# Performance work log

Hardware: AMD Instinct MI355X
Metric: run time of the kernel (lower is better)

## Reference

```python
import jax, jax.numpy as jnp
import numpy as np

SEQ_LEN = 256
VOCAB = 50000
EMBED = 300
PROJ = 200
ATT = 200
CLS = 3
B = 128


def setup_inputs() -> dict:
    key = jax.random.key(0)
    ks = jax.random.split(key, 16)
    s = lambda d: 1.0 / np.sqrt(d)
    return {
        "x1": jax.random.randint(ks[0], (B, SEQ_LEN), 0, VOCAB, dtype=jnp.int32),
        "x2": jax.random.randint(ks[1], (B, SEQ_LEN), 0, VOCAB, dtype=jnp.int32),
        "emb": jax.random.normal(ks[2], (VOCAB, EMBED), jnp.float32),
        # intra-attention forward_product FC (shared for x1/x2 via AUTO_REUSE)
        "Wi": jax.random.normal(ks[3], (EMBED, ATT), jnp.float32) * s(EMBED),
        "bi": jnp.zeros((ATT,), jnp.float32),
        "b_dist": jax.random.normal(ks[4], (1,), jnp.float32) * 0.1,
        # embed-scope projection (input is concat[x, xp] -> 2*EMBED), linear
        "Wp": jax.random.normal(ks[5], (2 * EMBED, PROJ), jnp.float32) * s(2 * EMBED),
        "bp": jnp.zeros((PROJ,), jnp.float32),
        # attent forward_product FC (shared)
        "Wa": jax.random.normal(ks[6], (PROJ, ATT), jnp.float32) * s(PROJ),
        "ba": jnp.zeros((ATT,), jnp.float32),
        # compare FC (shared, dim = input dim = 2*PROJ)
        "Wc": jax.random.normal(ks[7], (2 * PROJ, 2 * PROJ), jnp.float32) * s(2 * PROJ),
        "bc": jnp.zeros((2 * PROJ,), jnp.float32),
        # aggregate FC -> class logits (linear)
        "Wg": jax.random.normal(ks[8], (4 * PROJ, CLS), jnp.float32) * s(4 * PROJ),
        "bg": jnp.zeros((CLS,), jnp.float32),
    }


def _seq_mask(x):
    # tf.count_nonzero + tf.sequence_mask -> [B, L, 1] float mask
    size = jnp.sum((x != 0).astype(jnp.float32), axis=1)  # [B]
    m = (jnp.arange(SEQ_LEN)[None, :] < size[:, None]).astype(jnp.float32)
    return m[:, :, None]


def _intra(x, Wi, bi, b_dist):
    # forward_product on (x, x): relu FC then bilinear product -> [B, L, L]
    f = jax.nn.relu(x @ Wi + bi)
    att = jnp.einsum("bid,bjd->bij", f, f)
    idx = jnp.arange(SEQ_LEN)
    dist = jnp.abs(idx[None, :] - idx[:, None])
    bias = b_dist[0] * (dist >= 10).astype(jnp.float32)  # [L, L]
    xp = jnp.einsum("bik,bkj->bij", jax.nn.softmax(att + bias[None], axis=2), x)
    return jnp.concatenate([x, xp], axis=2)  # [B, L, 2*EMBED]


def reference(x1, x2, emb, Wi, bi, b_dist, Wp, bp, Wa, ba, Wc, bc, Wg, bg):
    mask1, mask2 = _seq_mask(x1), _seq_mask(x2)  # [B, L, 1]

    # embedding lookup with L2-normalized table
    emb_n = emb / jnp.linalg.norm(emb, axis=1, keepdims=True)
    e1, e2 = emb_n[x1], emb_n[x2]  # [B, L, EMBED]

    # intra-attention (distance-biased self alignment), doubles feature dim
    h1 = _intra(e1, Wi, bi, b_dist)
    h2 = _intra(e2, Wi, bi, b_dist)

    # linear projection to PROJ
    p1 = h1 @ Wp + bp  # [B, L, PROJ]
    p2 = h2 @ Wp + bp

    # attent: forward_product sim + mask + dual-axis softmax alignments
    a1 = jax.nn.relu(p1 @ Wa + ba)
    a2 = jax.nn.relu(p2 @ Wa + ba)
    sim = jnp.einsum("bid,bjd->bij", a1, a2)  # [B, L, L]
    sim = sim * (mask1 * jnp.swapaxes(mask2, 1, 2))
    alpha = jnp.einsum("bki,bkj->bij", jax.nn.softmax(sim, axis=1), p1)
    beta = jnp.einsum("bik,bkj->bij", jax.nn.softmax(sim, axis=2), p2)

    # compare (shared relu FC)
    v1 = jax.nn.relu(jnp.concatenate([p1, beta], 2) @ Wc + bc)
    v2 = jax.nn.relu(jnp.concatenate([p2, alpha], 2) @ Wc + bc)

    # aggregate: masked sum pooling + linear classifier
    v1 = jnp.sum(v1 * mask1, axis=1)  # [B, 2*PROJ]
    v2 = jnp.sum(v2 * mask2, axis=1)
    return jnp.concatenate([v1, v2], 1) @ Wg + bg  # [B, CLS]
```

## Files before the change

### kernel.cpp

```cpp
#include <hip/hip_runtime.h>
#include <math.h>

#define LSEQ 256
#define NB   128

typedef unsigned short u16;
typedef unsigned int   u32;
typedef __attribute__((ext_vector_type(8))) short bf16x8;
typedef __attribute__((ext_vector_type(4))) float f32x4;

static __device__ __forceinline__ u16 f2bf(float x) {
    union { float f; u32 u; } v; v.f = x;
    const u32 r = v.u + 0x7fffu + ((v.u >> 16) & 1u);
    return (u16)(r >> 16);
}
static __device__ __forceinline__ void glds16(const u16* src, u16* dst) {
    __builtin_amdgcn_global_load_lds(
        (const __attribute__((address_space(1))) u32*)src,
        (__attribute__((address_space(3))) u32*)dst, 16, 0, 0);
}

template<int EPI, bool BIAS, bool RELU>
__global__ __launch_bounds__(512)
void gemm(const u16* __restrict__ A, int lda,
          const u16* __restrict__ B, int ldb,
          u16* __restrict__ C, int ldc,
          const float* __restrict__ bias, int Nbias,
          float* __restrict__ pool, const float* __restrict__ pmask,
          int K, int Nwrite)
{
    __shared__ u16 As[128 * 64];
    __shared__ u16 Bs[256 * 64];

    const int m0 = blockIdx.y * 128;
    const int n0 = blockIdx.x * 256;
    const int t = threadIdx.x;
    const int lane = t & 63;
    const int w = t >> 6;
    const int wm = w >> 2;
    const int wn = w & 3;
    const int lr = lane & 15;
    const int lg = lane >> 4;

    f32x4 acc[4][4] = {};

    for (int k0 = 0; k0 < K; k0 += 64) {
#pragma unroll
        for (int i = 0; i < 2; ++i) {
            const int ch = w * 2 + i;
            const int row = (ch << 3) + (lane >> 3);
            const int slot = (lane & 7) ^ (row & 7);
            glds16(A + (long long)(m0 + row) * lda + k0 + (slot << 3), &As[ch << 9]);
        }
#pragma unroll
        for (int i = 0; i < 4; ++i) {
            const int ch = w * 4 + i;
            const int row = (ch << 3) + (lane >> 3);
            const int slot = (lane & 7) ^ (row & 7);
            glds16(B + (long long)(n0 + row) * ldb + k0 + (slot << 3), &Bs[ch << 9]);
        }
        __syncthreads();
#pragma unroll
        for (int kk = 0; kk < 2; ++kk) {
            bf16x8 af[4], bf[4];
#pragma unroll
            for (int mi = 0; mi < 4; ++mi) {
                const int row = wm * 64 + mi * 16 + lr;
                const int slot = ((kk << 2) + lg) ^ (row & 7);
                af[mi] = *reinterpret_cast<const bf16x8*>(&As[row * 64 + (slot << 3)]);
            }
#pragma unroll
            for (int ni = 0; ni < 4; ++ni) {
                const int row = wn * 64 + ni * 16 + lr;
                const int slot = ((kk << 2) + lg) ^ (row & 7);
                bf[ni] = *reinterpret_cast<const bf16x8*>(&Bs[row * 64 + (slot << 3)]);
            }
#pragma unroll
            for (int mi = 0; mi < 4; ++mi)
#pragma unroll
                for (int ni = 0; ni < 4; ++ni)
                    acc[mi][ni] = __builtin_amdgcn_mfma_f32_16x16x32_bf16(
                        af[mi], bf[ni], acc[mi][ni], 0, 0, 0);
        }
        __syncthreads();
    }

    const int rbase = lg << 2;
    if (EPI == 0) {
#pragma unroll
        for (int ni = 0; ni < 4; ++ni) {
            const int gc = n0 + wn * 64 + ni * 16 + lr;
            if (gc >= Nwrite) continue;
            float bcv = 0.f;
            if (BIAS) bcv = (gc < Nbias) ? bias[gc] : 0.f;
#pragma unroll
            for (int mi = 0; mi < 4; ++mi) {
#pragma unroll
                for (int r = 0; r < 4; ++r) {
                    const long long gr = m0 + wm * 64 + mi * 16 + rbase + r;
                    float x = acc[mi][ni][r];
                    if (BIAS) x += bcv;
                    if (RELU) x = fmaxf(x, 0.f);
                    C[gr * ldc + gc] = f2bf(x);
                }
            }
        }
    } else {
        __syncthreads();
        float* pool_s = reinterpret_cast<float*>(As);
        for (int i = t; i < 256; i += 512) pool_s[i] = 0.f;
        __syncthreads();
        const int b_lin = m0 >> 8;
        const int side  = b_lin >> 7;
        const int bb    = b_lin & 127;
        const float* mk = pmask + b_lin * 256 + (m0 & 255);
        float mrow[4][4];
#pragma unroll
        for (int mi = 0; mi < 4; ++mi)
#pragma unroll
            for (int r = 0; r < 4; ++r)
                mrow[mi][r] = mk[wm * 64 + mi * 16 + rbase + r];
#pragma unroll
        for (int ni = 0; ni < 4; ++ni) {
            const int lc = wn * 64 + ni * 16 + lr;
            const int gc = n0 + lc;
            const float bcv = (BIAS && gc < Nbias) ? bias[gc] : 0.f;
            float cs = 0.f;
#pragma unroll
            for (int mi = 0; mi < 4; ++mi)
#pragma unroll
                for (int r = 0; r < 4; ++r)
                    cs += fmaxf(acc[mi][ni][r] + bcv, 0.f) * mrow[mi][r];
            cs += __shfl_xor(cs, 16, 64);
            cs += __shfl_xor(cs, 32, 64);
            if (lg == 0) atomicAdd(&pool_s[lc], cs);
        }
        __syncthreads();
        for (int i = t; i < 256; i += 512) {
            const int gc = n0 + i;
            if (gc < Nwrite) atomicAdd(&pool[bb * 800 + side * 400 + gc], pool_s[i]);
        }
    }
}

template<int MODE>
__global__ __launch_bounds__(512)
void fattn(const u16* __restrict__ QK, u16* __restrict__ Hb,
           u16* __restrict__ CMP, u16* __restrict__ CMP2,
           const float* __restrict__ M1, const float* __restrict__ M2,
           const float* __restrict__ b_dist)
{
    constexpr int NVT = (MODE == 0) ? 5 : 4;
    __shared__ __align__(16) char shmem[16384 + NVT * 8192];
    u16* Pc = (u16*)shmem;
    u16* Vc = (u16*)(shmem + 16384);
    float* red  = (float*)shmem;
    float* red2 = red + 512;

    const int bz = blockIdx.x;
    int b, half, rowoff, ldv, ldc, Nwrite;
    const u16 *Kp, *Qp, *Vp;
    u16* Cp;
    const float *mrow = nullptr, *mcol = nullptr;
    if (MODE == 0) {
        b = (bz & 7) + (bz >> 4) * 8;
        half = (bz >> 3) & 1;
        Kp = QK + (long long)b * 65536;
        rowoff = half * 128;
        Qp = Kp + rowoff * 256;
        Vp = Hb + (long long)b * 163840; ldv = 640;
        Cp = Hb + (long long)b * 163840 + half * 128 * 640 + 320;
        ldc = 640; Nwrite = 320;
    } else {
        const int xcd = bz & 7, j = bz >> 3;
        const int sib = j & 3;
        b = xcd + (j >> 2) * 8;
        half = sib & 1;
        const int v = sib >> 1;
        const u16* a1 = QK + (long long)b * 65536;
        const u16* a2 = QK + 32768LL * 256 + (long long)b * 65536;
        u16* P1 = CMP  + (long long)b * 114688;
        u16* P2 = CMP2 + (long long)b * 114688;
        if (v == 0) { Qp = a1 + half * 128 * 256; Kp = a2; Vp = P2;
                      Cp = P1 + half * 128 * 448 + 200;
                      mrow = M1 + b * 256 + half * 128; mcol = M2 + b * 256; }
        else        { Qp = a2 + half * 128 * 256; Kp = a1; Vp = P1;
                      Cp = P2 + half * 128 * 448 + 200;
                      mrow = M2 + b * 256 + half * 128; mcol = M1 + b * 256; }
        ldv = 448; ldc = 448; Nwrite = 248; rowoff = 0;
    }

    const int t = threadIdx.x, lane = t & 63, w = t >> 6;
    const int lr = lane & 15, lg = lane >> 4;
    const int wk = w >> 1, wr = w & 1;
    const int wr2 = w >> 2, wc = w & 3;

    f32x4 acc[4][4] = {};
    for (int k0 = 0; k0 < 256; k0 += 64) {
#pragma unroll
        for (int kk = 0; kk < 2; ++kk) {
            const int ko = k0 + kk * 32 + lg * 8;
            bf16x8 kf[4], qf[4];
#pragma unroll
            for (int ki = 0; ki < 4; ++ki)
                kf[ki] = *reinterpret_cast<const bf16x8*>(
                    Kp + (long long)(wk * 64 + ki * 16 + lr) * 256 + ko);
#pragma unroll
            for (int qi = 0; qi < 4; ++qi)
                qf[qi] = *reinterpret_cast<const bf16x8*>(
                    Qp + (long long)(wr * 64 + qi * 16 + lr) * 256 + ko);
            __builtin_amdgcn_s_setprio(1);
#pragma unroll
            for (int ki = 0; ki < 4; ++ki)
#pragma unroll
                for (int qi = 0; qi < 4; ++qi)
                    acc[ki][qi] = __builtin_amdgcn_mfma_f32_16x16x32_bf16(
                        kf[ki], qf[qi], acc[ki][qi], 0, 0, 0);
            __builtin_amdgcn_s_setprio(0);
        }
    }

    if (MODE == 1) {
        float mr[4], mc[4][4];
#pragma unroll
        for (int qi = 0; qi < 4; ++qi) mr[qi] = mrow[wr * 64 + qi * 16 + lr];
#pragma unroll
        for (int ki = 0; ki < 4; ++ki)
#pragma unroll
            for (int r = 0; r < 4; ++r)
                mc[ki][r] = mcol[wk * 64 + ki * 16 + (lg << 2) + r];
#pragma unroll
        for (int ki = 0; ki < 4; ++ki)
#pragma unroll
            for (int qi = 0; qi < 4; ++qi)
#pragma unroll
                for (int r = 0; r < 4; ++r)
                    acc[ki][qi][r] *= mr[qi] * mc[ki][r];
    } else {
        const float bd = b_dist[0];
#pragma unroll
        for (int ki = 0; ki < 4; ++ki)
#pragma unroll
            for (int qi = 0; qi < 4; ++qi)
#pragma unroll
                for (int r = 0; r < 4; ++r) {
                    const int irow = rowoff + wr * 64 + qi * 16 + lr;
                    const int jcol = wk * 64 + ki * 16 + (lg << 2) + r;
                    const int d = irow > jcol ? irow - jcol : jcol - irow;
                    if (d >= 10) acc[ki][qi][r] += bd;
                }
    }

    const int n4  = (t & 63) << 2;
    const int k8v = (t >> 6) << 3;
    const int n4b = 256 + ((t & 15) << 2);
    const int k8b = (t >> 4) << 3;
    uint2 vreg[8], vtail[8];
#pragma unroll
    for (int i = 0; i < 8; ++i)
        vreg[i] = *reinterpret_cast<const uint2*>(Vp + (long long)(k8v + i) * ldv + n4);
    if (NVT == 5) {
        if (t < 128) {
#pragma unroll
            for (int i = 0; i < 8; ++i)
                vtail[i] = *reinterpret_cast<const uint2*>(Vp + (long long)(k8b + i) * ldv + n4b);
        }
    }

    float mx[4];
#pragma unroll
    for (int qi = 0; qi < 4; ++qi) {
        float m_ = -1e30f;
#pragma unroll
        for (int ki = 0; ki < 4; ++ki)
#pragma unroll
            for (int r = 0; r < 4; ++r) m_ = fmaxf(m_, acc[ki][qi][r]);
        m_ = fmaxf(m_, __shfl_xor(m_, 16, 64));
        m_ = fmaxf(m_, __shfl_xor(m_, 32, 64));
        mx[qi] = m_;
    }
    if (lg == 0) {
#pragma unroll
        for (int qi = 0; qi < 4; ++qi)
            red[(wr * 64 + qi * 16 + lr) * 4 + wk] = mx[qi];
    }
    __syncthreads();
    float sm[4];
#pragma unroll
    for (int qi = 0; qi < 4; ++qi) {
        const int row = wr * 64 + qi * 16 + lr;
        const float m_ = fmaxf(fmaxf(red[row * 4 + 0], red[row * 4 + 1]),
                               fmaxf(red[row * 4 + 2], red[row * 4 + 3]));
        float s_ = 0.f;
#pragma unroll
        for (int ki = 0; ki < 4; ++ki)
#pragma unroll
            for (int r = 0; r < 4; ++r) {
                const float e_ = __expf(acc[ki][qi][r] - m_);
                acc[ki][qi][r] = e_;
                s_ += e_;
            }
        s_ += __shfl_xor(s_, 16, 64);
        s_ += __shfl_xor(s_, 32, 64);
        sm[qi] = s_;
    }
    if (lg == 0) {
#pragma unroll
        for (int qi = 0; qi < 4; ++qi)
            red2[(wr * 64 + qi * 16 + lr) * 4 + wk] = sm[qi];
    }
    __syncthreads();
#pragma unroll
    for (int qi = 0; qi < 4; ++qi) {
        const int row = wr * 64 + qi * 16 + lr;
        const float rs = 1.0f / (red2[row * 4 + 0] + red2[row * 4 + 1]
                               + red2[row * 4 + 2] + red2[row * 4 + 3]);
#pragma unroll
        for (int ki = 0; ki < 4; ++ki)
#pragma unroll
            for (int r = 0; r < 4; ++r) acc[ki][qi][r] *= rs;
    }
    __syncthreads();

    f32x4 opv[4][NVT] = {};
    for (int c = 0; c < 4; ++c) {
        {
            union { uint2 q2[8]; u16 s[32]; } uq;
#pragma unroll
            for (int i = 0; i < 8; ++i) uq.q2[i] = vreg[i];
#pragma unroll
            for (int j = 0; j < 4; ++j) {
                const int row = n4 + j;
                const u32 v0 = (u32)uq.s[j]      | ((u32)uq.s[4 + j]  << 16);
                const u32 v1 = (u32)uq.s[8 + j]  | ((u32)uq.s[12 + j] << 16);
                const u32 v2 = (u32)uq.s[16 + j] | ((u32)uq.s[20 + j] << 16);
                const u32 v3 = (u32)uq.s[24 + j] | ((u32)uq.s[28 + j] << 16);
                const int slot = (t >> 6) ^ (row & 7);
                *reinterpret_cast<uint4*>(&Vc[row * 64 + (slot << 3)]) =
                    make_uint4(v0, v1, v2, v3);
            }
            if (NVT == 5 && t < 128) {
                union { uint2 q2[8]; u16 s[32]; } ub;
#pragma unroll
                for (int i = 0; i < 8; ++i) ub.q2[i] = vtail[i];
#pragma unroll
                for (int j = 0; j < 4; ++j) {
                    const int row = n4b + j;
                    const u32 v0 = (u32)ub.s[j]      | ((u32)ub.s[4 + j]  << 16);
                    const u32 v1 = (u32)ub.s[8 + j]  | ((u32)ub.s[12 + j] << 16);
                    const u32 v2 = (u32)ub.s[16 + j] | ((u32)ub.s[20 + j] << 16);
                    const u32 v3 = (u32)ub.s[24 + j] | ((u32)ub.s[28 + j] << 16);
                    const int slot = (t >> 4) ^ (row & 7);
                    *reinterpret_cast<uint4*>(&Vc[row * 64 + (slot << 3)]) =
                        make_uint4(v0, v1, v2, v3);
                }
            }
        }
        if (wk == c) {
#pragma unroll
            for (int qi = 0; qi < 4; ++qi) {
                const int qrow = wr * 64 + qi * 16 + lr;
#pragma unroll
                for (int ki = 0; ki < 4; ++ki) {
                    const u32 lo = (u32)f2bf(acc[ki][qi][0]) | ((u32)f2bf(acc[ki][qi][1]) << 16);
                    const u32 hi = (u32)f2bf(acc[ki][qi][2]) | ((u32)f2bf(acc[ki][qi][3]) << 16);
                    const int slot = ((ki << 1) + (lg >> 1)) ^ (qrow & 7);
                    *reinterpret_cast<uint2*>(
                        (char*)Pc + qrow * 128 + (slot << 4) + ((lg & 1) << 3)) =
                        make_uint2(lo, hi);
                }
            }
        }
        if (c < 3) {
#pragma unroll
            for (int i = 0; i < 8; ++i)
                vreg[i] = *reinterpret_cast<const uint2*>(
                    Vp + (long long)((c + 1) * 64 + k8v + i) * ldv + n4);
            if (NVT == 5 && t < 128) {
#pragma unroll
                for (int i = 0; i < 8; ++i)
                    vtail[i] = *reinterpret_cast<const uint2*>(
                        Vp + (long long)((c + 1) * 64 + k8b + i) * ldv + n4b);
            }
        }
        __syncthreads();
#pragma unroll
        for (int kk = 0; kk < 2; ++kk) {
            bf16x8 pa[4], vb[NVT];
#pragma unroll
            for (int qi = 0; qi < 4; ++qi) {
                const int row = wr2 * 64 + qi * 16 + lr;
                const int slot = ((kk << 2) + lg) ^ (row & 7);
                pa[qi] = *reinterpret_cast<const bf16x8*>(&Pc[row * 64 + (slot << 3)]);
            }
#pragma unroll
            for (int vi = 0; vi < NVT; ++vi) {
                const int row = wc * (NVT * 16) + vi * 16 + lr;
                const int slot = ((kk << 2) + lg) ^ (row & 7);
                vb[vi] = *reinterpret_cast<const bf16x8*>(&Vc[row * 64 + (slot << 3)]);
            }
            __builtin_amdgcn_s_setprio(1);
#pragma unroll
            for (int qi = 0; qi < 4; ++qi)
#pragma unroll
                for (int vi = 0; vi < NVT; ++vi)
                    opv[qi][vi] = __builtin_amdgcn_mfma_f32_16x16x32_bf16(
                        pa[qi], vb[vi], opv[qi][vi], 0, 0, 0);
            __builtin_amdgcn_s_setprio(0);
        }
        __syncthreads();
    }

#pragma unroll
    for (int qi = 0; qi < 4; ++qi)
#pragma unroll
        for (int vi = 0; vi < NVT; ++vi) {
            const int gc = wc * (NVT * 16) + vi * 16 + lr;
            if (gc >= Nwrite) continue;
#pragma unroll
            for (int r = 0; r < 4; ++r) {
                const int qrow = wr2 * 64 + qi * 16 + (lg << 2) + r;
                Cp[(long long)qrow * ldc + gc] = f2bf(opv[qi][vi][r]);
            }
        }
}

__global__ __launch_bounds__(256)
void prep_small(const int* __restrict__ x1, const int* __restrict__ x2,
                float* __restrict__ M1f, float* __restrict__ POOL)
{
    const int blk = blockIdx.x;
    const int b = blk & 127;
    const int t = threadIdx.x;
    const int* x = (blk < 128) ? x1 : x2;
    float* mask = M1f + (blk < 128 ? 0 : 32768);
    int nz = (x[b * LSEQ + t] != 0) ? 1 : 0;
#pragma unroll
    for (int o = 32; o; o >>= 1) nz += __shfl_xor(nz, o, 64);
    __shared__ int red[4];
    if ((t & 63) == 0) red[t >> 6] = nz;
    __syncthreads();
    const int size = red[0] + red[1] + red[2] + red[3];
    mask[b * LSEQ + t] = (t < size) ? 1.0f : 0.0f;
    if (blk < 128) {
        for (int i = t; i < 800; i += 256) POOL[b * 800 + i] = 0.f;
    }
}

__global__ __launch_bounds__(256)
void prep_weights(const float* __restrict__ Wi, const float* __restrict__ Wa,
                  const float* __restrict__ Wp, const float* __restrict__ Wc,
                  u16* __restrict__ WiT, u16* __restrict__ WaT,
                  u16* __restrict__ WpT, u16* __restrict__ WcT)
{
    int idx = blockIdx.x * 256 + threadIdx.x;
    const float* src; u16* dst; int srcRows, srcCols, dstCols, seg1, seg2;
    if (idx < 81920)       { src = Wi; dst = WiT; srcRows = 300; srcCols = 200; dstCols = 320; seg1 = 300; seg2 = 320; }
    else if (idx < 147456) { idx -= 81920;  src = Wa; dst = WaT; srcRows = 200; srcCols = 200; dstCols = 256; seg1 = 200; seg2 = 256; }
    else if (idx < 311296) { idx -= 147456; src = Wp; dst = WpT; srcRows = 600; srcCols = 200; dstCols = 640; seg1 = 300; seg2 = 320; }
    else                   { idx -= 311296; src = Wc; dst = WcT; srcRows = 400; srcCols = 400; dstCols = 448; seg1 = 400; seg2 = 448; }
    const int n = idx / dstCols, k = idx - n * dstCols;
    int sr = -1;
    if (k < seg1) sr = k;
    else if (k >= seg2 && (k - seg2) < (srcRows - seg1)) sr = seg1 + (k - seg2);
    u16 v = 0;
    if (n < srcCols && sr >= 0) v = f2bf(src[(long long)sr * srcCols + n]);
    dst[idx] = v;
}

__global__ __launch_bounds__(256)
void gather_norm(const int* __restrict__ x1, const int* __restrict__ x2,
                 const float* __restrict__ emb, u16* __restrict__ h)
{
    const int t = threadIdx.x;
    const int lane = t & 63;
    const long long row = (long long)blockIdx.x * 4 + (t >> 6);
    const int tok = (row < 32768) ? x1[row] : x2[row - 32768];
    const float* er = emb + (long long)tok * 300;
    float vals[5];
    float ss = 0.f;
#pragma unroll
    for (int i = 0; i < 5; ++i) {
        const int c = lane + i * 64;
        const float v = (c < 300) ? er[c] : 0.f;
        vals[i] = v;
        ss = fmaf(v, v, ss);
    }
#pragma unroll
    for (int o = 32; o; o >>= 1) ss += __shfl_xor(ss, o, 64);
    const float inv = 1.0f / sqrtf(ss);
    u16* out = h + row * 640;
#pragma unroll
    for (int i = 0; i < 5; ++i) {
        const int c = lane + i * 64;
        out[c] = f2bf(vals[i] * inv);
    }
}

__global__ __launch_bounds__(256)
void final_fc(const float* __restrict__ pooled, const float* __restrict__ Wg,
              const float* __restrict__ bg, float* __restrict__ out)
{
    const int b = blockIdx.x;
    const int t = threadIdx.x;
    float a0 = 0.f, a1 = 0.f, a2 = 0.f;
    for (int k = t; k < 800; k += 256) {
        const float p = pooled[(long long)b * 800 + k];
        a0 = fmaf(p, Wg[k * 3 + 0], a0);
        a1 = fmaf(p, Wg[k * 3 + 1], a1);
        a2 = fmaf(p, Wg[k * 3 + 2], a2);
    }
#pragma unroll
    for (int o = 32; o; o >>= 1) {
        a0 += __shfl_xor(a0, o, 64);
        a1 += __shfl_xor(a1, o, 64);
        a2 += __shfl_xor(a2, o, 64);
    }
    __shared__ float r0[4], r1[4], r2[4];
    if ((t & 63) == 0) { r0[t >> 6] = a0; r1[t >> 6] = a1; r2[t >> 6] = a2; }
    __syncthreads();
    if (t == 0) {
        out[b * 3 + 0] = r0[0] + r0[1] + r0[2] + r0[3] + bg[0];
        out[b * 3 + 1] = r1[0] + r1[1] + r1[2] + r1[3] + bg[1];
        out[b * 3 + 2] = r2[0] + r2[1] + r2[2] + r2[3] + bg[2];
    }
}

extern "C" void kernel_launch(void* const* d_in, const int* in_sizes, int n_in,
                              void* d_out, int out_size, void* d_ws, size_t ws_size,
                              hipStream_t stream)
{
    (void)in_sizes; (void)n_in; (void)out_size; (void)ws_size;

    const int*   x1     = (const int*)  d_in[0];
    const int*   x2     = (const int*)  d_in[1];
    const float* emb    = (const float*)d_in[2];
    const float* Wi     = (const float*)d_in[3];
    const float* bi     = (const float*)d_in[4];
    const float* b_dist = (const float*)d_in[5];
    const float* Wp     = (const float*)d_in[6];
    const float* bp     = (const float*)d_in[7];
    const float* Wa     = (const float*)d_in[8];
    const float* ba     = (const float*)d_in[9];
    const float* Wc     = (const float*)d_in[10];
    const float* bc     = (const float*)d_in[11];
    const float* Wg     = (const float*)d_in[12];
    const float* bg     = (const float*)d_in[13];
    float* out = (float*)d_out;

    u16* wsu  = (u16*)d_ws;
    u16* H    = wsu;
    u16* CMP  = wsu + 41943040;
    u16* FA   = wsu + 71303168;
    u16* WiT  = wsu + 88080384;
    u16* WaT  = wsu + 88162304;
    u16* WpT  = wsu + 88227840;
    u16* WcT  = wsu + 88391680;
    float* fb = (float*)(wsu + 88621056);
    float* POOL = fb;
    float* M1f  = fb + 102400;
    float* M2f  = fb + 135168;

    u16* CMP2 = CMP + (long long)32768 * 448;

    prep_small<<<256, 256, 0, stream>>>(x1, x2, M1f, POOL);
    prep_weights<<<2112, 256, 0, stream>>>(Wi, Wa, Wp, Wc, WiT, WaT, WpT, WcT);
    gather_norm<<<16384, 256, 0, stream>>>(x1, x2, emb, H);

    gemm<0, true, true><<<dim3(1, 512, 1), 512, 0, stream>>>(
        H, 640, WiT, 320, FA, 256, bi, 200, nullptr, nullptr, 320, 256);
    fattn<0><<<512, 512, 0, stream>>>(FA, H, nullptr, nullptr, nullptr, nullptr, b_dist);
    gemm<0, true, false><<<dim3(1, 512, 1), 512, 0, stream>>>(
        H, 640, WpT, 640, CMP, 448, bp, 200, nullptr, nullptr, 640, 256);
    gemm<0, true, true><<<dim3(1, 512, 1), 512, 0, stream>>>(
        CMP, 448, WaT, 256, FA, 256, ba, 200, nullptr, nullptr, 256, 256);
    fattn<1><<<512, 512, 0, stream>>>(FA, nullptr, CMP, CMP2, M1f, M2f, nullptr);
    gemm<2, true, true><<<dim3(2, 512, 1), 512, 0, stream>>>(
        CMP, 448, WcT, 448, nullptr, 0, bc, 400, POOL, M1f, 448, 400);

    final_fc<<<NB, 256, 0, stream>>>(POOL, Wg, bg, out);
}
```

Baseline: 244.8 us.

## Stage attention QK tiles through double-buffered LDS and merge prep kernels

In the attention kernel, K and Q tiles now go through swizzled, double-buffered shared memory using async global-to-LDS loads, prefetching the next 32-wide k slice while MFMAs run on the current one. Before, each wave read fragments straight from global memory. In self-attention mode Q reuses the K buffer, since both come from the same matrix. The three prep kernels (mask/pool init, weight transpose, embedding gather) are also merged into one launch to cut launch overhead. The cost is a larger shared-memory footprint, which can lower occupancy, plus an extra barrier per k step.

```diff
diff --git a/kernel.cpp b/kernel.cpp
--- a/kernel.cpp
+++ b/kernel.cpp
@@ -151,7 +151,11 @@
            const float* __restrict__ b_dist)
 {
     constexpr int NVT = (MODE == 0) ? 5 : 4;
-    __shared__ __align__(16) char shmem[16384 + NVT * 8192];
+    __shared__ __align__(16) char shmem[MODE == 0 ? 57344 : 49152];
+    u16* Ks0 = (u16*)shmem;
+    u16* Ks1 = (u16*)(shmem + 16384);
+    u16* Qs0 = (u16*)(shmem + 32768);
+    u16* Qs1 = (u16*)(shmem + 40960);
     u16* Pc = (u16*)shmem;
     u16* Vc = (u16*)(shmem + 16384);
     float* red  = (float*)shmem;
@@ -166,11 +170,10 @@
         b = (bz & 7) + (bz >> 4) * 8;
         half = (bz >> 3) & 1;
         Kp = QK + (long long)b * 65536;
-        rowoff = half * 128;
-        Qp = Kp + rowoff * 256;
+        Qp = Kp;
         Vp = Hb + (long long)b * 163840; ldv = 640;
         Cp = Hb + (long long)b * 163840 + half * 128 * 640 + 320;
-        ldc = 640; Nwrite = 320;
+        ldc = 640; Nwrite = 320; rowoff = half * 128;
     } else {
         const int xcd = bz & 7, j = bz >> 3;
         const int sib = j & 3;
@@ -196,19 +199,48 @@
     const int wr2 = w >> 2, wc = w & 3;
 
     f32x4 acc[4][4] = {};
-    for (int k0 = 0; k0 < 256; k0 += 64) {
-#pragma unroll
-        for (int kk = 0; kk < 2; ++kk) {
-            const int ko = k0 + kk * 32 + lg * 8;
+    {
+        const int krow = (lane >> 2);
+        const int kslot = (lane & 3) ^ (krow & 3);
+#pragma unroll
+        for (int i = 0; i < 2; ++i) {
+            const int ch = w * 2 + i;
+            glds16(Kp + (long long)(ch * 16 + krow) * 256 + (kslot << 3), Ks0 + (ch << 9));
+        }
+        if (MODE != 0)
+            glds16(Qp + (long long)(w * 16 + krow) * 256 + (kslot << 3), Qs0 + (w << 9));
+        __syncthreads();
+        for (int it = 0; it < 8; ++it) {
+            if (it < 7) {
+                const int k0 = (it + 1) * 32;
+                u16* kb = ((it + 1) & 1) ? Ks1 : Ks0;
+#pragma unroll
+                for (int i = 0; i < 2; ++i) {
+                    const int ch = w * 2 + i;
+                    glds16(Kp + (long long)(ch * 16 + krow) * 256 + k0 + (kslot << 3),
+                           kb + (ch << 9));
+                }
+                if (MODE != 0) {
+                    u16* qb = ((it + 1) & 1) ? Qs1 : Qs0;
+                    glds16(Qp + (long long)(w * 16 + krow) * 256 + k0 + (kslot << 3),
+                           qb + (w << 9));
+                }
+            }
+            const u16* kb = (it & 1) ? Ks1 : Ks0;
+            const u16* qb = (MODE == 0) ? kb : ((it & 1) ? Qs1 : Qs0);
             bf16x8 kf[4], qf[4];
 #pragma unroll
-            for (int ki = 0; ki < 4; ++ki)
+            for (int ki = 0; ki < 4; ++ki) {
+                const int row = wk * 64 + ki * 16 + lr;
                 kf[ki] = *reinterpret_cast<const bf16x8*>(
-                    Kp + (long long)(wk * 64 + ki * 16 + lr) * 256 + ko);
-#pragma unroll
-            for (int qi = 0; qi < 4; ++qi)
+                    &kb[row * 32 + ((lg ^ (row & 3)) << 3)]);
+            }
+#pragma unroll
+            for (int qi = 0; qi < 4; ++qi) {
+                const int row = (MODE == 0 ? rowoff : 0) + wr * 64 + qi * 16 + lr;
                 qf[qi] = *reinterpret_cast<const bf16x8*>(
-                    Qp + (long long)(wr * 64 + qi * 16 + lr) * 256 + ko);
+                    &qb[row * 32 + ((lg ^ (row & 3)) << 3)]);
+            }
             __builtin_amdgcn_s_setprio(1);
 #pragma unroll
             for (int ki = 0; ki < 4; ++ki)
@@ -217,6 +249,7 @@
                     acc[ki][qi] = __builtin_amdgcn_mfma_f32_16x16x32_bf16(
                         kf[ki], qf[qi], acc[ki][qi], 0, 0, 0);
             __builtin_amdgcn_s_setprio(0);
+            __syncthreads();
         }
     }
 
@@ -426,74 +459,70 @@
 }
 
 __global__ __launch_bounds__(256)
-void prep_small(const int* __restrict__ x1, const int* __restrict__ x2,
-                float* __restrict__ M1f, float* __restrict__ POOL)
+void prep_all(const int* __restrict__ x1, const int* __restrict__ x2,
+              const float* __restrict__ emb,
+              const float* __restrict__ Wi, const float* __restrict__ Wa,
+              const float* __restrict__ Wp, const float* __restrict__ Wc,
+              u16* __restrict__ h,
+              u16* __restrict__ WiT, u16* __restrict__ WaT,
+              u16* __restrict__ WpT, u16* __restrict__ WcT,
+              float* __restrict__ M1f, float* __restrict__ POOL)
 {
     const int blk = blockIdx.x;
-    const int b = blk & 127;
     const int t = threadIdx.x;
-    const int* x = (blk < 128) ? x1 : x2;
-    float* mask = M1f + (blk < 128 ? 0 : 32768);
-    int nz = (x[b * LSEQ + t] != 0) ? 1 : 0;
-#pragma unroll
-    for (int o = 32; o; o >>= 1) nz += __shfl_xor(nz, o, 64);
-    __shared__ int red[4];
-    if ((t & 63) == 0) red[t >> 6] = nz;
-    __syncthreads();
-    const int size = red[0] + red[1] + red[2] + red[3];
-    mask[b * LSEQ + t] = (t < size) ? 1.0f : 0.0f;
-    if (blk < 128) {
-        for (int i = t; i < 800; i += 256) POOL[b * 800 + i] = 0.f;
-    }
-}
-
-__global__ __launch_bounds__(256)
-void prep_weights(const float* __restrict__ Wi, const float* __restrict__ Wa,
-                  const float* __restrict__ Wp, const float* __restrict__ Wc,
-                  u16* __restrict__ WiT, u16* __restrict__ WaT,
-                  u16* __restrict__ WpT, u16* __restrict__ WcT)
-{
-    int idx = blockIdx.x * 256 + threadIdx.x;
-    const float* src; u16* dst; int srcRows, srcCols, dstCols, seg1, seg2;
-    if (idx < 81920)       { src = Wi; dst = WiT; srcRows = 300; srcCols = 200; dstCols = 320; seg1 = 300; seg2 = 320; }
-    else if (idx < 147456) { idx -= 81920;  src = Wa; dst = WaT; srcRows = 200; srcCols = 200; dstCols = 256; seg1 = 200; seg2 = 256; }
-    else if (idx < 311296) { idx -= 147456; src = Wp; dst = WpT; srcRows = 600; srcCols = 200; dstCols = 640; seg1 = 300; seg2 = 320; }
-    else                   { idx -= 311296; src = Wc; dst = WcT; srcRows = 400; srcCols = 400; dstCols = 448; seg1 = 400; seg2 = 448; }
-    const int n = idx / dstCols, k = idx - n * dstCols;
-    int sr = -1;
-    if (k < seg1) sr = k;
-    else if (k >= seg2 && (k - seg2) < (srcRows - seg1)) sr = seg1 + (k - seg2);
-    u16 v = 0;
-    if (n < srcCols && sr >= 0) v = f2bf(src[(long long)sr * srcCols + n]);
-    dst[idx] = v;
-}
-
-__global__ __launch_bounds__(256)
-void gather_norm(const int* __restrict__ x1, const int* __restrict__ x2,
-                 const float* __restrict__ emb, u16* __restrict__ h)
-{
-    const int t = threadIdx.x;
-    const int lane = t & 63;
-    const long long row = (long long)blockIdx.x * 4 + (t >> 6);
-    const int tok = (row < 32768) ? x1[row] : x2[row - 32768];
-    const float* er = emb + (long long)tok * 300;
-    float vals[5];
-    float ss = 0.f;
-#pragma unroll
-    for (int i = 0; i < 5; ++i) {
-        const int c = lane + i * 64;
-        const float v = (c < 300) ? er[c] : 0.f;
-        vals[i] = v;
-        ss = fmaf(v, v, ss);
-    }
-#pragma unroll
-    for (int o = 32; o; o >>= 1) ss += __shfl_xor(ss, o, 64);
-    const float inv = 1.0f / sqrtf(ss);
-    u16* out = h + row * 640;
-#pragma unroll
-    for (int i = 0; i < 5; ++i) {
-        const int c = lane + i * 64;
-        out[c] = f2bf(vals[i] * inv);
+    if (blk < 16384) {
+        const int lane = t & 63;
+        const long long row = (long long)blk * 4 + (t >> 6);
+        const int tok = (row < 32768) ? x1[row] : x2[row - 32768];
+        const float* er = emb + (long long)tok * 300;
+        float vals[5];
+        float ss = 0.f;
+#pragma unroll
+        for (int i = 0; i < 5; ++i) {
+            const int c = lane + i * 64;
+            const float v = (c < 300) ? er[c] : 0.f;
+            vals[i] = v;
+            ss = fmaf(v, v, ss);
+        }
+#pragma unroll
+        for (int o = 32; o; o >>= 1) ss += __shfl_xor(ss, o, 64);
+        const float inv = 1.0f / sqrtf(ss);
+        u16* outp = h + row * 640;
+#pragma unroll
+        for (int i = 0; i < 5; ++i) {
+            const int c = lane + i * 64;
+            outp[c] = f2bf(vals[i] * inv);
+        }
+    } else if (blk < 18496) {
+        int idx = (blk - 16384) * 256 + t;
+        const float* src; u16* dst; int srcRows, srcCols, dstCols, seg1, seg2;
+        if (idx < 81920)       { src = Wi; dst = WiT; srcRows = 300; srcCols = 200; dstCols = 320; seg1 = 300; seg2 = 320; }
+        else if (idx < 147456) { idx -= 81920;  src = Wa; dst = WaT; srcRows = 200; srcCols = 200; dstCols = 256; seg1 = 200; seg2 = 256; }
+        else if (idx < 311296) { idx -= 147456; src = Wp; dst = WpT; srcRows = 600; srcCols = 200; dstCols = 640; seg1 = 300; seg2 = 320; }
+        else                   { idx -= 311296; src = Wc; dst = WcT; srcRows = 400; srcCols = 400; dstCols = 448; seg1 = 400; seg2 = 448; }
+        const int n = idx / dstCols, k = idx - n * dstCols;
+        int sr = -1;
+        if (k < seg1) sr = k;
+        else if (k >= seg2 && (k - seg2) < (srcRows - seg1)) sr = seg1 + (k - seg2);
+        u16 v = 0;
+        if (n < srcCols && sr >= 0) v = f2bf(src[(long long)sr * srcCols + n]);
+        dst[idx] = v;
+    } else {
+        const int b2 = blk - 18496;
+        const int b = b2 & 127;
+        const int* x = (b2 < 128) ? x1 : x2;
+        float* mask = M1f + (b2 < 128 ? 0 : 32768);
+        int nz = (x[b * LSEQ + t] != 0) ? 1 : 0;
+#pragma unroll
+        for (int o = 32; o; o >>= 1) nz += __shfl_xor(nz, o, 64);
+        __shared__ int red[4];
+        if ((t & 63) == 0) red[t >> 6] = nz;
+        __syncthreads();
+        const int size = red[0] + red[1] + red[2] + red[3];
+        mask[b * LSEQ + t] = (t < size) ? 1.0f : 0.0f;
+        if (b2 < 128) {
+            for (int i = t; i < 800; i += 256) POOL[b * 800 + i] = 0.f;
+        }
     }
 }
 
@@ -563,9 +592,8 @@
 
     u16* CMP2 = CMP + (long long)32768 * 448;
 
-    prep_small<<<256, 256, 0, stream>>>(x1, x2, M1f, POOL);
-    prep_weights<<<2112, 256, 0, stream>>>(Wi, Wa, Wp, Wc, WiT, WaT, WpT, WcT);
-    gather_norm<<<16384, 256, 0, stream>>>(x1, x2, emb, H);
+    prep_all<<<18752, 256, 0, stream>>>(x1, x2, emb, Wi, Wa, Wp, Wc,
+                                        H, WiT, WaT, WpT, WcT, M1f, POOL);
 
     gemm<0, true, true><<<dim3(1, 512, 1), 512, 0, stream>>>(
         H, 640, WiT, 320, FA, 256, bi, 200, nullptr, nullptr, 320, 256);
```

New measurement: 201.4 us. 17.7% less time.
